# Optimization experiments

Measured on AMD Instinct MI355X. Metric: run time of the kernel, lower is better.

## Reference

```python
import jax, jax.numpy as jnp
import numpy as np

EPS = 1e-5        # BatchNorm eps (torch default)
SLOPE = 0.2       # LeakyReLU negative slope
K_DIL, K_DIL_POS, K = 8, 6, 32


def _sqdist(a):
    # a: (B,N,D) -> squared pairwise distances (B,N,N); monotone in cdist(p=2)
    n = jnp.sum(a * a, axis=-1)
    return n[:, :, None] + n[:, None, :] - 2.0 * jnp.einsum('bnd,bmd->bnm', a, a)


def _knn(a, k):
    # k nearest neighbors excluding self (drop the closest = self, as in torch topk[..., 1:])
    _, idx = jax.lax.top_k(-_sqdist(a), k + 1)
    return idx[:, :, 1:]  # (B,N,k) int32


def _edge_feat(x, idx):
    # x: (B,N,C), idx: (B,N,K) -> (B,N,K,2C) = concat(neighbor - center, center)
    B = x.shape[0]
    b_idx = jnp.arange(B)[:, None, None]
    nbr = x[b_idx, idx]                       # (B,N,K,C) gather
    ctr = x[:, :, None, :]                    # (B,N,1,C)
    ctr_b = jnp.broadcast_to(ctr, nbr.shape)
    return jnp.concatenate([nbr - ctr, ctr_b], axis=-1)


def _conv_bn_lrelu(f, W, g, b):
    # 1x1 Conv2d (no bias) + BatchNorm2d(track_running_stats=False, batch stats) + LeakyReLU(0.2)
    # f: (B,N,K,Cin), W: (Cout,Cin)
    y = jnp.einsum('bnkc,oc->bnko', f, W)
    mu = jnp.mean(y, axis=(0, 1, 2))
    var = jnp.var(y, axis=(0, 1, 2))          # biased var, as torch BN normalization
    y = (y - mu) * jax.lax.rsqrt(var + EPS) * g + b
    return jnp.where(y > 0, y, SLOPE * y)


def setup_inputs() -> dict:
    key = jax.random.key(0)
    ks = jax.random.split(key, 8)
    B, N, C, D = 2, 4096, 64, 3
    hidden, out_c = 128, 64
    c1 = 2 * C   # convdilated channels
    c2 = 4 * C   # conv input channels (edge feature of 2C-dim features)
    return {
        'x': jax.random.normal(ks[0], (B, N, C), jnp.float32),
        'pos': jax.random.normal(ks[1], (B, N, D), jnp.float32),
        'W1': jax.random.normal(ks[2], (c1, c1), jnp.float32) * 0.05,
        'g1': jnp.ones((c1,), jnp.float32),
        'b1': jnp.zeros((c1,), jnp.float32),
        'W2': jax.random.normal(ks[3], (hidden, c2), jnp.float32) * 0.05,
        'g2': jnp.ones((hidden,), jnp.float32),
        'b2': jnp.zeros((hidden,), jnp.float32),
        'W3': jax.random.normal(ks[4], (out_c, hidden), jnp.float32) * 0.05,
        'g3': jnp.ones((out_c,), jnp.float32),
        'b3': jnp.zeros((out_c,), jnp.float32),
    }


def reference(x, pos, W1, g1, b1, W2, g2, b2, W3, g3, b3):
    # Dual graph 1: feature-KNN (k_dilated) concat pos-KNN (k_dilated_pos)
    idx1 = jnp.concatenate([_knn(x, K_DIL), _knn(pos, K_DIL_POS)], axis=2)  # (B,N,14)
    f1 = _edge_feat(x, idx1)                                                # (B,N,14,2C)
    h1 = jnp.max(_conv_bn_lrelu(f1, W1, g1, b1), axis=2)                    # (B,N,2C)
    # Graph 2: k_pos == 0 -> pure position KNN
    idx2 = _knn(pos, K)                                                     # (B,N,32)
    f2 = _edge_feat(h1, idx2)                                               # (B,N,32,4C)
    h2 = _conv_bn_lrelu(f2, W2, g2, b2)                                     # (B,N,32,hidden)
    h3 = _conv_bn_lrelu(h2, W3, g3, b3)                                     # (B,N,32,out)
    out = jnp.max(h3, axis=2)                                               # (B,N,out)
    return out, idx2
```

## Files before the change

### kernel.cpp

```cpp
#include <hip/hip_runtime.h>
#include <hip/hip_bf16.h>
#include <type_traits>

using bf16 = __hip_bfloat16;

namespace {

constexpr int B_ = 2;
constexpr int N_ = 4096;
constexpr int C_ = 64;
constexpr int K14_ = 14;
constexpr int KX_ = 8;
constexpr int KP_ = 6;
constexpr int K2_ = 32;
constexpr int OC_ = 64;

__device__ __forceinline__ float bflo(unsigned u) { return __uint_as_float(u << 16); }
__device__ __forceinline__ float bfhi(unsigned u) { return __uint_as_float(u & 0xffff0000u); }

__device__ __forceinline__ unsigned pack_f16(float a, float b) {
  _Float16 ha = (_Float16)a, hb = (_Float16)b;
  unsigned short ua = __builtin_bit_cast(unsigned short, ha);
  unsigned short ub = __builtin_bit_cast(unsigned short, hb);
  return (unsigned)ua | ((unsigned)ub << 16);
}

using half2v = __attribute__((ext_vector_type(2))) _Float16;
__device__ __forceinline__ float dot2(unsigned a, unsigned b, float acc) {
#if __has_builtin(__builtin_amdgcn_fdot2)
  return __builtin_amdgcn_fdot2(__builtin_bit_cast(half2v, a),
                                __builtin_bit_cast(half2v, b), acc, false);
#else
  half2v ha = __builtin_bit_cast(half2v, a), hb = __builtin_bit_cast(half2v, b);
  acc = fmaf((float)ha[0], (float)hb[0], acc);
  return fmaf((float)ha[1], (float)hb[1], acc);
#endif
}

__device__ __forceinline__ unsigned fmono(float d) {
  unsigned u = __float_as_uint(d);
  return u ^ (((int)u < 0) ? 0xFFFFFFFFu : 0x80000000u);
}

#define GRP8_ONE(GV, GS, T) \
  { bool av = !((taken >> (T)) & 1ull); bool bb = av && dst[T] < GV; \
    GV = bb ? dst[T] : GV; GS = bb ? (T) : GS; }
#define GRP8(GV, GS, B) do { GV = 3.0e38f; GS = B; \
  GRP8_ONE(GV, GS, (B)+0) GRP8_ONE(GV, GS, (B)+1) GRP8_ONE(GV, GS, (B)+2) \
  GRP8_ONE(GV, GS, (B)+3) GRP8_ONE(GV, GS, (B)+4) GRP8_ONE(GV, GS, (B)+5) \
  GRP8_ONE(GV, GS, (B)+6) GRP8_ONE(GV, GS, (B)+7) } while (0)
#define GTREE_ONE(GV, GS) { bool bb = GV < pv; pv = bb ? GV : pv; ptt = bb ? GS : ptt; }
#define GTREE() do { pv = gv0; ptt = gs0; \
  GTREE_ONE(gv1, gs1) GTREE_ONE(gv2, gs2) GTREE_ONE(gv3, gs3) GTREE_ONE(gv4, gs4) \
  GTREE_ONE(gv5, gs5) GTREE_ONE(gv6, gs6) GTREE_ONE(gv7, gs7) } while (0)
#define GRP_SWITCH(TT) do { switch ((TT) >> 3) { \
  case 0: GRP8(gv0, gs0, 0);  break; case 1: GRP8(gv1, gs1, 8);  break; \
  case 2: GRP8(gv2, gs2, 16); break; case 3: GRP8(gv3, gs3, 24); break; \
  case 4: GRP8(gv4, gs4, 32); break; case 5: GRP8(gv5, gs5, 40); break; \
  case 6: GRP8(gv6, gs6, 48); break; case 7: GRP8(gv7, gs7, 56); break; } \
  GTREE(); } while (0)
#define SEL_DECL float gv0, gv1, gv2, gv3, gv4, gv5, gv6, gv7; \
  int gs0, gs1, gs2, gs3, gs4, gs5, gs6, gs7; float pv; int ptt; \
  unsigned long long taken = 0ull;
#define SEL_INIT do { \
  GRP8(gv0, gs0, 0);  GRP8(gv1, gs1, 8);  GRP8(gv2, gs2, 16); GRP8(gv3, gs3, 24); \
  GRP8(gv4, gs4, 32); GRP8(gv5, gs5, 40); GRP8(gv6, gs6, 48); GRP8(gv7, gs7, 56); \
  GTREE(); } while (0)

__global__ __launch_bounds__(256)
void xnorm_kernel(const float* __restrict__ x, float* __restrict__ nx)
{
  int p = blockIdx.x * 256 + threadIdx.x;
  if (p >= B_ * N_) return;
  float s = 0.f;
#pragma unroll 8
  for (int c = 0; c < C_; ++c) { float v = x[p * C_ + c]; s = fmaf(v, v, s); }
  nx[p] = s;
}

__global__ __launch_bounds__(256)
void wprep_kernel(const float* __restrict__ W1, const float* __restrict__ W2,
                  const float* __restrict__ W3,
                  float* __restrict__ WT1a, float* __restrict__ WT1bm,
                  float* __restrict__ WT2a, float* __restrict__ WT2bm,
                  unsigned* __restrict__ w3p)
{
  int idx = blockIdx.x * 256 + threadIdx.x;
  if (idx < 128 * 128) {
    int o = idx & 127, c = idx >> 7;
    float a = W2[o * 256 + c];
    WT2a[c * 128 + o] = a;
    WT2bm[c * 128 + o] = W2[o * 256 + 128 + c] - a;
    if (c < 64) {
      float a1 = W1[o * 128 + c];
      WT1a[c * 128 + o] = a1;
      WT1bm[c * 128 + o] = W1[o * 128 + 64 + c] - a1;
    }
  }
  if (idx < 64 * 64) {
    int oo = idx & 63, c2 = idx >> 6;
    w3p[c2 * 64 + oo] = pack_f16(W3[oo * 128 + 2 * c2], W3[oo * 128 + 2 * c2 + 1]);
  }
}

__global__ __launch_bounds__(512, 4)
void knn_x_kernel(const float* __restrict__ x, const float* __restrict__ nx,
                  int* __restrict__ idx1)
{
  __shared__ unsigned tileh[256 * 33];
  const int wave = threadIdx.x >> 6, lane = threadIdx.x & 63;
  const int qg = blockIdx.x * 8 + wave;
  const int bb = qg >> 12;
  const float* xb = x + bb * N_ * C_;
  unsigned myq;
  {
    float2 qv = *(const float2*)&x[qg * C_ + 2 * (lane & 31)];
    myq = pack_f16(qv.x, qv.y);
  }
  unsigned qp[32];
#pragma unroll
  for (int c2 = 0; c2 < 32; ++c2) qp[c2] = __builtin_amdgcn_readlane(myq, c2);
  const float nq = nx[qg];
  const float* nb_ = nx + bb * N_;
  float dst[64];
#pragma unroll
  for (int ti = 0; ti < 16; ++ti) {
    __syncthreads();
    for (int e = threadIdx.x; e < 256 * 32; e += 512) {
      int c2 = e & 31, j = e >> 5;
      float2 v = *(const float2*)&xb[(ti * 256 + j) * C_ + 2 * c2];
      tileh[j * 33 + c2] = pack_f16(v.x, v.y);
    }
    __syncthreads();
#pragma unroll
    for (int nb4 = 0; nb4 < 4; ++nb4) {
      const unsigned* row = &tileh[(nb4 * 64 + lane) * 33];
      float acc = 0.f;
#pragma unroll
      for (int c2 = 0; c2 < 32; ++c2) acc = dot2(qp[c2], row[c2], acc);
      float nbv = nb_[ti * 256 + nb4 * 64 + lane];
      dst[ti * 4 + nb4] = nq + nbv - 2.f * acc;
    }
  }
  SEL_DECL;
  SEL_INIT;
  for (int r = 0; r < KX_ + 1; ++r) {
    int j = ((ptt >> 2) << 8) + ((ptt & 3) << 6) + lane;
    unsigned long long key = ((unsigned long long)fmono(pv) << 32) | (unsigned)j;
#pragma unroll
    for (int m = 1; m < 64; m <<= 1) {
      unsigned long long ok = __shfl_xor(key, m, 64);
      key = ok < key ? ok : key;
    }
    int wj = (int)(key & 0xFFFFFFFFull);
    if (r > 0 && lane == 0) idx1[qg * K14_ + (r - 1)] = wj;
    if ((wj & 63) == lane) {
      int tt = ((wj >> 8) << 2) | ((wj >> 6) & 3);
      taken |= 1ull << tt;
      GRP_SWITCH(tt);
    }
  }
}

__global__ __launch_bounds__(512, 2)
void knn_pos_kernel(const float* __restrict__ pos,
                    int* __restrict__ idx1, int* __restrict__ idx2,
                    float* __restrict__ oidx)
{
#pragma clang fp contract(off)
  __shared__ float pL[3][N_];
  __shared__ float nL[N_];
  const int wave = threadIdx.x >> 6, lane = threadIdx.x & 63;
  const int qg = blockIdx.x * 8 + wave;
  const int bb = qg >> 12;
  const float* pb = pos + bb * N_ * 3;
  for (int j = threadIdx.x; j < N_; j += 512) {
    float a = pb[j * 3], b = pb[j * 3 + 1], c = pb[j * 3 + 2];
    pL[0][j] = a; pL[1][j] = b; pL[2][j] = c;
    float aa = a * a;
    float bb2 = b * b;
    float cc = c * c;
    float s1 = aa + bb2;
    nL[j] = s1 + cc;
  }
  __syncthreads();
  const int q = qg & (N_ - 1);
  const float qx = pL[0][q], qy = pL[1][q], qz = pL[2][q];
  const float nq = nL[q];
  float dst[64];
#pragma unroll
  for (int t = 0; t < 64; ++t) {
    int j = t * 64 + lane;
    float dot = qx * pL[0][j];
    dot = fmaf(qy, pL[1][j], dot);
    dot = fmaf(qz, pL[2][j], dot);
    float t1 = nq + nL[j];
    float t2 = 2.0f * dot;
    dst[t] = t1 - t2;
  }
  SEL_DECL;
  SEL_INIT;
  for (int r = 0; r < K2_ + 1; ++r) {
    int j = ptt * 64 + lane;
    unsigned long long key = ((unsigned long long)fmono(pv) << 32) | (unsigned)j;
#pragma unroll
    for (int m = 1; m < 64; m <<= 1) {
      unsigned long long ok = __shfl_xor(key, m, 64);
      key = ok < key ? ok : key;
    }
    int wj = (int)(key & 0xFFFFFFFFull);
    if (r > 0 && lane == 0) {
      int rr = r - 1;
      if (rr < KP_) idx1[qg * K14_ + KX_ + rr] = wj;
      idx2[qg * K2_ + rr] = wj;
      oidx[qg * K2_ + rr] = (float)wj;
    }
    if ((wj & 63) == lane) {
      int tt = wj >> 6;
      taken |= 1ull << tt;
      GRP_SWITCH(tt);
    }
  }
}

template<int CIN, typename TIN>
__global__ __launch_bounds__(256)
void lin_kernel(const TIN* __restrict__ in, const float* __restrict__ WT,
                bf16* __restrict__ out)
{
  __shared__ float wt[CIN * 128];
  for (int e = threadIdx.x; e < CIN * 128; e += 256) wt[e] = WT[e];
  __syncthreads();
  const int which = threadIdx.x >> 7, o = threadIdx.x & 127;
  for (int p0 = blockIdx.x * 2; p0 < B_ * N_; p0 += gridDim.x * 2) {
    int p = p0 + which;
    float acc = 0.f;
#pragma unroll 8
    for (int c = 0; c < CIN; ++c) {
      float v;
      if constexpr (std::is_same_v<TIN, float>) v = in[p * CIN + c];
      else v = __bfloat162float(in[p * CIN + c]);
      acc = fmaf(wt[c * 128 + o], v, acc);
    }
    out[p * 128 + o] = __float2bfloat16(acc);
  }
}

template<int KNB>
__global__ __launch_bounds__(256)
void stats_gather_kernel(const bf16* __restrict__ a, const bf16* __restrict__ ac,
                         const int* __restrict__ nbr, double* __restrict__ st)
{
  const int o = threadIdx.x & 127;
  const int which = threadIdx.x >> 7;
  double s = 0.0, s2 = 0.0;
  for (int p0 = blockIdx.x * 2; p0 < B_ * N_; p0 += gridDim.x * 2) {
    int p = p0 + which;
    int base = (p >> 12) << 12;
    float acv = __bfloat162float(ac[p * 128 + o]);
#pragma unroll 2
    for (int kk = 0; kk < KNB; ++kk) {
      int nb = nbr[p * KNB + kk] & (N_ - 1);
      float y = __bfloat162float(a[(base + nb) * 128 + o]) + acv;
      s += (double)y; s2 += (double)y * (double)y;
    }
  }
  atomicAdd(&st[o], s);
  atomicAdd(&st[128 + o], s2);
}

__global__ void bnfin_kernel(const double* __restrict__ st, const float* __restrict__ g,
                             const float* __restrict__ bi, float* __restrict__ so,
                             int nch, double cnt)
{
  int o = threadIdx.x;
  if (o >= nch) return;
  double mu = st[o] / cnt;
  double var = st[nch + o] / cnt - mu * mu;
  double sc = (double)g[o] / sqrt(var + 1e-5);
  so[o] = (float)sc;
  so[nch + o] = (float)((double)bi[o] - mu * sc);
}

__global__ __launch_bounds__(256)
void h1_kernel(const bf16* __restrict__ u, const bf16* __restrict__ uc,
               const int* __restrict__ idx1, const float* __restrict__ so,
               bf16* __restrict__ h1)
{
  const int o = threadIdx.x & 127, which = threadIdx.x >> 7;
  float sc = so[o], off = so[128 + o];
  for (int p0 = blockIdx.x * 2; p0 < B_ * N_; p0 += gridDim.x * 2) {
    int p = p0 + which;
    int base = (p >> 12) << 12;
    float ucv = __bfloat162float(uc[p * 128 + o]);
    float m = -3.0e38f;
#pragma unroll
    for (int kk = 0; kk < K14_; ++kk) {
      int nb = idx1[p * K14_ + kk] & (N_ - 1);
      float y = __bfloat162float(u[(base + nb) * 128 + o]) + ucv;
      float v = fmaf(y, sc, off);
      v = v > 0.f ? v : 0.2f * v;
      m = fmaxf(m, v);
    }
    h1[p * 128 + o] = __float2bfloat16(m);
  }
}

template<int PASS>
__global__ __launch_bounds__(256, 5)
void conv3_kernel(const bf16* __restrict__ z, const bf16* __restrict__ zc,
                  const int* __restrict__ idx2, const float* __restrict__ so2,
                  const float* __restrict__ so3, const unsigned* __restrict__ w3p,
                  double* __restrict__ st3, float* __restrict__ outp)
{
  __shared__ unsigned w3s[64 * 64];
  __shared__ unsigned h2s[4][512];
  {
    const uint4* src = (const uint4*)w3p;
    uint4* dst4 = (uint4*)w3s;
    for (int e = threadIdx.x; e < 1024; e += 256) dst4[e] = src[e];
  }
  __syncthreads();
  const int wave = threadIdx.x >> 6, lane = threadIdx.x & 63;
  unsigned* h2w = &h2s[wave][0];
  const int swz = (lane >> 2) & 7;
  const float sclo = so2[2 * lane],       schi = so2[2 * lane + 1];
  const float offlo = so2[128 + 2 * lane], offhi = so2[129 + 2 * lane];
  float sc3 = 0.f, off3 = 0.f;
  if constexpr (PASS == 1) { sc3 = so3[lane]; off3 = so3[64 + lane]; }
  double s = 0.0, s2 = 0.0;
  const int gw = blockIdx.x * 4 + wave;
  const int stride = gridDim.x * 4;
  for (int p = gw; p < B_ * N_; p += stride) {
    const int base = (p >> 12) << 12;
    const unsigned zcv = *(const unsigned*)&zc[p * 128 + 2 * lane];
    const float zclo = bflo(zcv), zchi = bfhi(zcv);
    float m = -3.0e38f;
#pragma unroll
    for (int kc = 0; kc < 4; ++kc) {
      asm volatile("s_waitcnt lgkmcnt(0)" ::: "memory");
#pragma unroll
      for (int i = 0; i < 8; ++i) {
        int nb = idx2[p * K2_ + kc * 8 + i] & (N_ - 1);
        unsigned zv = *(const unsigned*)&z[(base + nb) * 128 + 2 * lane];
        float y0 = bflo(zv) + zclo;
        float y1 = bfhi(zv) + zchi;
        float v0 = fmaf(y0, sclo, offlo); v0 = v0 > 0.f ? v0 : 0.2f * v0;
        float v1 = fmaf(y1, schi, offhi); v1 = v1 > 0.f ? v1 : 0.2f * v1;
        h2w[(lane << 3) | (i ^ swz)] = pack_f16(v0, v1);
      }
      asm volatile("s_waitcnt lgkmcnt(0)" ::: "memory");
      float a0 = 0.f, a1 = 0.f, a2 = 0.f, a3 = 0.f;
      float a4 = 0.f, a5 = 0.f, a6 = 0.f, a7 = 0.f;
#pragma unroll
      for (int c2 = 0; c2 < 64; ++c2) {
        const int cs = (c2 >> 2) & 7;
        unsigned wp = w3s[(c2 << 6) | lane];
        uint4 ra = *(const uint4*)&h2w[c2 << 3];
        uint4 rb = *(const uint4*)&h2w[(c2 << 3) + 4];
        unsigned hv[8] = {ra.x, ra.y, ra.z, ra.w, rb.x, rb.y, rb.z, rb.w};
        a0 = dot2(wp, hv[0 ^ cs], a0);
        a1 = dot2(wp, hv[1 ^ cs], a1);
        a2 = dot2(wp, hv[2 ^ cs], a2);
        a3 = dot2(wp, hv[3 ^ cs], a3);
        a4 = dot2(wp, hv[4 ^ cs], a4);
        a5 = dot2(wp, hv[5 ^ cs], a5);
        a6 = dot2(wp, hv[6 ^ cs], a6);
        a7 = dot2(wp, hv[7 ^ cs], a7);
      }
      if constexpr (PASS == 0) {
        s += (double)a0 + (double)a1 + (double)a2 + (double)a3
           + (double)a4 + (double)a5 + (double)a6 + (double)a7;
        s2 += (double)a0 * a0 + (double)a1 * a1 + (double)a2 * a2 + (double)a3 * a3
            + (double)a4 * a4 + (double)a5 * a5 + (double)a6 * a6 + (double)a7 * a7;
      } else {
        float v;
        v = fmaf(a0, sc3, off3); v = v > 0.f ? v : 0.2f * v; m = fmaxf(m, v);
        v = fmaf(a1, sc3, off3); v = v > 0.f ? v : 0.2f * v; m = fmaxf(m, v);
        v = fmaf(a2, sc3, off3); v = v > 0.f ? v : 0.2f * v; m = fmaxf(m, v);
        v = fmaf(a3, sc3, off3); v = v > 0.f ? v : 0.2f * v; m = fmaxf(m, v);
        v = fmaf(a4, sc3, off3); v = v > 0.f ? v : 0.2f * v; m = fmaxf(m, v);
        v = fmaf(a5, sc3, off3); v = v > 0.f ? v : 0.2f * v; m = fmaxf(m, v);
        v = fmaf(a6, sc3, off3); v = v > 0.f ? v : 0.2f * v; m = fmaxf(m, v);
        v = fmaf(a7, sc3, off3); v = v > 0.f ? v : 0.2f * v; m = fmaxf(m, v);
      }
    }
    if constexpr (PASS == 1) outp[p * OC_ + lane] = m;
  }
  if constexpr (PASS == 0) {
    atomicAdd(&st3[lane], s);
    atomicAdd(&st3[64 + lane], s2);
  }
}

}

extern "C" void kernel_launch(void* const* d_in, const int* in_sizes, int n_in,
                              void* d_out, int out_size, void* d_ws, size_t ws_size,
                              hipStream_t stream) {
  const float* x   = (const float*)d_in[0];
  const float* pos = (const float*)d_in[1];
  const float* W1  = (const float*)d_in[2];
  const float* g1  = (const float*)d_in[3];
  const float* b1  = (const float*)d_in[4];
  const float* W2  = (const float*)d_in[5];
  const float* g2  = (const float*)d_in[6];
  const float* b2  = (const float*)d_in[7];
  const float* W3  = (const float*)d_in[8];
  const float* g3  = (const float*)d_in[9];
  const float* b3  = (const float*)d_in[10];

  float* outp = (float*)d_out;
  float* oidx = outp + B_ * N_ * OC_;

  char* w = (char*)d_ws;
  double* stats = (double*)w;            w += 640 * sizeof(double);
  float* nxf    = (float*)w;             w += B_ * N_ * 4;
  float* WT1a   = (float*)w;             w += 64 * 128 * 4;
  float* WT1bm  = (float*)w;             w += 64 * 128 * 4;
  float* WT2a   = (float*)w;             w += 128 * 128 * 4;
  float* WT2bm  = (float*)w;             w += 128 * 128 * 4;
  unsigned* w3p = (unsigned*)w;          w += 64 * 64 * 4;
  float* so1    = (float*)w;             w += 256 * 4;
  float* so2    = (float*)w;             w += 256 * 4;
  float* so3    = (float*)w;             w += 128 * 4;
  int* idx1     = (int*)w;               w += B_ * N_ * K14_ * 4;
  int* idx2i    = (int*)w;               w += B_ * N_ * K2_ * 4;
  bf16* u       = (bf16*)w;              w += B_ * N_ * 128 * 2;
  bf16* uc      = (bf16*)w;              w += B_ * N_ * 128 * 2;
  bf16* h1      = (bf16*)w;              w += B_ * N_ * 128 * 2;
  bf16* zz  = u;
  bf16* zzc = uc;

  hipMemsetAsync(stats, 0, 640 * sizeof(double), stream);

  xnorm_kernel<<<(B_ * N_ + 255) / 256, 256, 0, stream>>>(x, nxf);
  wprep_kernel<<<64, 256, 0, stream>>>(W1, W2, W3, WT1a, WT1bm, WT2a, WT2bm, w3p);

  knn_x_kernel<<<1024, 512, 0, stream>>>(x, nxf, idx1);
  knn_pos_kernel<<<1024, 512, 0, stream>>>(pos, idx1, idx2i, oidx);

  lin_kernel<64, float><<<2048, 256, 0, stream>>>(x, WT1a, u);
  lin_kernel<64, float><<<2048, 256, 0, stream>>>(x, WT1bm, uc);

  stats_gather_kernel<K14_><<<2048, 256, 0, stream>>>(u, uc, idx1, stats);
  bnfin_kernel<<<1, 128, 0, stream>>>(stats, g1, b1, so1, 128, (double)(B_ * N_ * K14_));
  h1_kernel<<<2048, 256, 0, stream>>>(u, uc, idx1, so1, h1);

  lin_kernel<128, bf16><<<2048, 256, 0, stream>>>(h1, WT2a, zz);
  lin_kernel<128, bf16><<<2048, 256, 0, stream>>>(h1, WT2bm, zzc);

  stats_gather_kernel<K2_><<<2048, 256, 0, stream>>>(zz, zzc, idx2i, stats + 256);
  bnfin_kernel<<<1, 128, 0, stream>>>(stats + 256, g2, b2, so2, 128, (double)(B_ * N_ * K2_));

  conv3_kernel<0><<<2048, 256, 0, stream>>>(zz, zzc, idx2i, so2, nullptr, w3p, stats + 512, nullptr);
  bnfin_kernel<<<1, 128, 0, stream>>>(stats + 512, g3, b3, so3, 64, (double)(B_ * N_ * K2_));
  conv3_kernel<1><<<2048, 256, 0, stream>>>(zz, zzc, idx2i, so2, so3, w3p, nullptr, outp);
}
```

Baseline: 822.1 us.

## Replace second conv3 pass with per-channel max/min tracking and cheap finalize

The stats pass now also records the per-point, per-channel max and min of the pre-BN conv3 outputs, packed as fp16 pairs. A small elementwise finalize kernel then picks max or min according to the sign of the BN scale and applies the affine transform and LeakyReLU. This works because the activation is monotone, and it removes a second full gather plus matmul pass over all 32 neighbors. In exchange, the extremes are stored in fp16, which loses precision, and the grid size of the stats kernel is halved.

New measurement: 698.6 us. 1.18x faster.

```diff
diff --git a/kernel.cpp b/kernel.cpp
--- a/kernel.cpp
+++ b/kernel.cpp
@@ -306,12 +306,11 @@
   }
 }
 
-template<int PASS>
 __global__ __launch_bounds__(256, 5)
-void conv3_kernel(const bf16* __restrict__ z, const bf16* __restrict__ zc,
-                  const int* __restrict__ idx2, const float* __restrict__ so2,
-                  const float* __restrict__ so3, const unsigned* __restrict__ w3p,
-                  double* __restrict__ st3, float* __restrict__ outp)
+void conv3s_kernel(const bf16* __restrict__ z, const bf16* __restrict__ zc,
+                   const int* __restrict__ idx2, const float* __restrict__ so2,
+                   const unsigned* __restrict__ w3p,
+                   double* __restrict__ st3, unsigned* __restrict__ y3m)
 {
   __shared__ unsigned w3s[64 * 64];
   __shared__ unsigned h2s[4][512];
@@ -326,8 +325,6 @@
   const int swz = (lane >> 2) & 7;
   const float sclo = so2[2 * lane],       schi = so2[2 * lane + 1];
   const float offlo = so2[128 + 2 * lane], offhi = so2[129 + 2 * lane];
-  float sc3 = 0.f, off3 = 0.f;
-  if constexpr (PASS == 1) { sc3 = so3[lane]; off3 = so3[64 + lane]; }
   double s = 0.0, s2 = 0.0;
   const int gw = blockIdx.x * 4 + wave;
   const int stride = gridDim.x * 4;
@@ -335,7 +332,7 @@
     const int base = (p >> 12) << 12;
     const unsigned zcv = *(const unsigned*)&zc[p * 128 + 2 * lane];
     const float zclo = bflo(zcv), zchi = bfhi(zcv);
-    float m = -3.0e38f;
+    float mx = -3.0e38f, mn = 3.0e38f;
 #pragma unroll
     for (int kc = 0; kc < 4; ++kc) {
       asm volatile("s_waitcnt lgkmcnt(0)" ::: "memory");
@@ -368,29 +365,33 @@
         a6 = dot2(wp, hv[6 ^ cs], a6);
         a7 = dot2(wp, hv[7 ^ cs], a7);
       }
-      if constexpr (PASS == 0) {
-        s += (double)a0 + (double)a1 + (double)a2 + (double)a3
-           + (double)a4 + (double)a5 + (double)a6 + (double)a7;
-        s2 += (double)a0 * a0 + (double)a1 * a1 + (double)a2 * a2 + (double)a3 * a3
-            + (double)a4 * a4 + (double)a5 * a5 + (double)a6 * a6 + (double)a7 * a7;
-      } else {
-        float v;
-        v = fmaf(a0, sc3, off3); v = v > 0.f ? v : 0.2f * v; m = fmaxf(m, v);
-        v = fmaf(a1, sc3, off3); v = v > 0.f ? v : 0.2f * v; m = fmaxf(m, v);
-        v = fmaf(a2, sc3, off3); v = v > 0.f ? v : 0.2f * v; m = fmaxf(m, v);
-        v = fmaf(a3, sc3, off3); v = v > 0.f ? v : 0.2f * v; m = fmaxf(m, v);
-        v = fmaf(a4, sc3, off3); v = v > 0.f ? v : 0.2f * v; m = fmaxf(m, v);
-        v = fmaf(a5, sc3, off3); v = v > 0.f ? v : 0.2f * v; m = fmaxf(m, v);
-        v = fmaf(a6, sc3, off3); v = v > 0.f ? v : 0.2f * v; m = fmaxf(m, v);
-        v = fmaf(a7, sc3, off3); v = v > 0.f ? v : 0.2f * v; m = fmaxf(m, v);
-      }
-    }
-    if constexpr (PASS == 1) outp[p * OC_ + lane] = m;
-  }
-  if constexpr (PASS == 0) {
-    atomicAdd(&st3[lane], s);
-    atomicAdd(&st3[64 + lane], s2);
-  }
+      s += (double)a0 + (double)a1 + (double)a2 + (double)a3
+         + (double)a4 + (double)a5 + (double)a6 + (double)a7;
+      s2 += (double)a0 * a0 + (double)a1 * a1 + (double)a2 * a2 + (double)a3 * a3
+          + (double)a4 * a4 + (double)a5 * a5 + (double)a6 * a6 + (double)a7 * a7;
+      mx = fmaxf(mx, fmaxf(fmaxf(a0, a1), fmaxf(a2, a3)));
+      mx = fmaxf(mx, fmaxf(fmaxf(a4, a5), fmaxf(a6, a7)));
+      mn = fminf(mn, fminf(fminf(a0, a1), fminf(a2, a3)));
+      mn = fminf(mn, fminf(fminf(a4, a5), fminf(a6, a7)));
+    }
+    y3m[p * OC_ + lane] = pack_f16(mx, mn);
+  }
+  atomicAdd(&st3[lane], s);
+  atomicAdd(&st3[64 + lane], s2);
+}
+
+__global__ __launch_bounds__(256)
+void fin3_kernel(const unsigned* __restrict__ y3m, const float* __restrict__ so3,
+                 float* __restrict__ outp)
+{
+  int idx = blockIdx.x * 256 + threadIdx.x;
+  if (idx >= B_ * N_ * OC_) return;
+  int oo = idx & 63;
+  float sc3 = so3[oo], off3 = so3[64 + oo];
+  half2v hv = __builtin_bit_cast(half2v, y3m[idx]);
+  float pick = (sc3 >= 0.f) ? (float)hv[0] : (float)hv[1];
+  float v = fmaf(pick, sc3, off3);
+  outp[idx] = v > 0.f ? v : 0.2f * v;
 }
 
 }
@@ -431,6 +432,7 @@
   bf16* h1      = (bf16*)w;              w += B_ * N_ * 128 * 2;
   bf16* zz  = u;
   bf16* zzc = uc;
+  unsigned* y3m = (unsigned*)h1;
 
   hipMemsetAsync(stats, 0, 640 * sizeof(double), stream);
 
@@ -453,7 +455,7 @@
   stats_gather_kernel<K2_><<<2048, 256, 0, stream>>>(zz, zzc, idx2i, stats + 256);
   bnfin_kernel<<<1, 128, 0, stream>>>(stats + 256, g2, b2, so2, 128, (double)(B_ * N_ * K2_));
 
-  conv3_kernel<0><<<2048, 256, 0, stream>>>(zz, zzc, idx2i, so2, nullptr, w3p, stats + 512, nullptr);
+  conv3s_kernel<<<1024, 256, 0, stream>>>(zz, zzc, idx2i, so2, w3p, stats + 512, y3m);
   bnfin_kernel<<<1, 128, 0, stream>>>(stats + 512, g3, b3, so3, 64, (double)(B_ * N_ * K2_));
-  conv3_kernel<1><<<2048, 256, 0, stream>>>(zz, zzc, idx2i, so2, so3, w3p, nullptr, outp);
-}
+  fin3_kernel<<<B_ * N_ * OC_ / 256, 256, 0, stream>>>(y3m, so3, outp);
+}
```
